# Kernel optimization log

Measured on AMD Instinct MI355X. Metric: run time of the kernel, lower is better.

The kernel has to match this reference:

```python
import jax, jax.numpy as jnp
import numpy as np

EPS = 1e-7  # keras backend epsilon


def _tril_indices(stack_size: int) -> np.ndarray:
    # matches np.nonzero(np.tri(S, S, -1).ravel())[0] in build()
    return np.nonzero(np.tri(stack_size, stack_size, -1).ravel())[0]


def setup_inputs() -> dict:
    key = jax.random.key(0)
    x = jax.random.normal(key, (8, 512, 256), dtype=jnp.float32)
    return {"x": x}


def reference(x) -> jnp.ndarray:
    B, S, D = x.shape
    tril = jnp.asarray(_tril_indices(S))  # static, length S*(S-1)/2
    # pairwise squared L2 over feature dim: (B, S, S, D) -> (B, S, S)
    diff = x[:, :, None, :] - x[:, None, :, :]
    d2 = jnp.sum(jnp.square(diff), axis=-1)
    d = jnp.sqrt(jnp.maximum(d2, EPS))
    # flatten the S x S matrix and gather strict lower-triangular entries
    out = d.reshape(B, S * S)[:, tril]  # (B, S*(S-1)/2)
    return out
```

## Files before the change

kernel.cpp:

```cpp
#include <hip/hip_runtime.h>
#include <hip/hip_bf16.h>
#include <math.h>

#define BB 8
#define SS 512
#define DD 256
#define PP (SS * (SS - 1) / 2)
#define TILES_PER_B (32 * 33 / 2)

typedef short bf16x8 __attribute__((ext_vector_type(8)));
typedef float f32x4 __attribute__((ext_vector_type(4)));

static __device__ inline unsigned short f2bf(float f) {
    unsigned int u = __float_as_uint(f);
    unsigned int r = u + 0x7fffu + ((u >> 16) & 1u);
    return (unsigned short)(r >> 16);
}

__global__ __launch_bounds__(256) void prep_kernel(const float* __restrict__ x,
                                                   unsigned short* __restrict__ xb,
                                                   float* __restrict__ norms) {
    int row  = blockIdx.x * 4 + (threadIdx.x >> 6);
    int lane = threadIdx.x & 63;
    const float4* src = reinterpret_cast<const float4*>(x + (size_t)row * DD) + lane;
    float4 v = *src;
    float ss = v.x * v.x + v.y * v.y + v.z * v.z + v.w * v.w;
    ushort4 pk;
    pk.x = f2bf(v.x); pk.y = f2bf(v.y); pk.z = f2bf(v.z); pk.w = f2bf(v.w);
    *reinterpret_cast<ushort4*>(xb + (size_t)row * DD + lane * 4) = pk;
    #pragma unroll
    for (int o = 32; o > 0; o >>= 1) ss += __shfl_down(ss, o);
    if (lane == 0) norms[row] = ss;
}

__global__ __launch_bounds__(256) void dist_kernel(const unsigned short* __restrict__ xb,
                                                   const float* __restrict__ norms,
                                                   float* __restrict__ out) {
    int w    = blockIdx.x * 4 + (threadIdx.x >> 6);
    int lane = threadIdx.x & 63;
    int b    = w / TILES_PER_B;
    int tidx = w - b * TILES_PER_B;
    int ti = (int)((sqrtf(8.0f * (float)tidx + 1.0f) - 1.0f) * 0.5f);
    while ((ti + 1) * (ti + 2) / 2 <= tidx) ti++;
    while (ti * (ti + 1) / 2 > tidx) ti--;
    int tj = tidx - ti * (ti + 1) / 2;

    int nidx = lane & 15;
    int quad = lane >> 4;

    const unsigned short* arow = xb + ((size_t)(b * SS + ti * 16 + nidx)) * DD + quad * 8;
    const unsigned short* brow = xb + ((size_t)(b * SS + tj * 16 + nidx)) * DD + quad * 8;

    f32x4 acc = {0.f, 0.f, 0.f, 0.f};
    #pragma unroll
    for (int k = 0; k < DD; k += 32) {
        bf16x8 av = *reinterpret_cast<const bf16x8*>(arow + k);
        bf16x8 bv = *reinterpret_cast<const bf16x8*>(brow + k);
        acc = __builtin_amdgcn_mfma_f32_16x16x32_bf16(av, bv, acc, 0, 0, 0);
    }

    int jg = tj * 16 + nidx;
    float nj = norms[b * SS + jg];
    float* outb = out + (size_t)b * PP;
    #pragma unroll
    for (int r = 0; r < 4; r++) {
        int ig = ti * 16 + quad * 4 + r;
        if (ig > jg) {
            float ni = norms[b * SS + ig];
            float d2 = ni + nj - 2.0f * acc[r];
            d2 = fmaxf(d2, 1e-7f);
            outb[(size_t)(ig * (ig - 1) / 2) + jg] = sqrtf(d2);
        }
    }
}

extern "C" void kernel_launch(void* const* d_in, const int* in_sizes, int n_in,
                              void* d_out, int out_size, void* d_ws, size_t ws_size,
                              hipStream_t stream) {
    const float* x = (const float*)d_in[0];
    float* out = (float*)d_out;
    unsigned short* xb = (unsigned short*)d_ws;
    float* norms = (float*)((char*)d_ws + (size_t)BB * SS * DD * 2);

    prep_kernel<<<1024, 256, 0, stream>>>(x, xb, norms);
    dist_kernel<<<1056, 256, 0, stream>>>(xb, norms, out);
}
```

Before: 68.63 us.

## Fuse bf16 conversion and norm computation into distance kernel

```diff
diff --git a/kernel.cpp b/kernel.cpp
--- a/kernel.cpp
+++ b/kernel.cpp
@@ -1,5 +1,4 @@
 #include <hip/hip_runtime.h>
-#include <hip/hip_bf16.h>
 #include <math.h>
 
 #define BB 8
@@ -17,25 +16,22 @@
     return (unsigned short)(r >> 16);
 }
 
-__global__ __launch_bounds__(256) void prep_kernel(const float* __restrict__ x,
-                                                   unsigned short* __restrict__ xb,
-                                                   float* __restrict__ norms) {
-    int row  = blockIdx.x * 4 + (threadIdx.x >> 6);
-    int lane = threadIdx.x & 63;
-    const float4* src = reinterpret_cast<const float4*>(x + (size_t)row * DD) + lane;
-    float4 v = *src;
-    float ss = v.x * v.x + v.y * v.y + v.z * v.z + v.w * v.w;
-    ushort4 pk;
-    pk.x = f2bf(v.x); pk.y = f2bf(v.y); pk.z = f2bf(v.z); pk.w = f2bf(v.w);
-    *reinterpret_cast<ushort4*>(xb + (size_t)row * DD + lane * 4) = pk;
-    #pragma unroll
-    for (int o = 32; o > 0; o >>= 1) ss += __shfl_down(ss, o);
-    if (lane == 0) norms[row] = ss;
+static __device__ inline bf16x8 cvt8(float4 a0, float4 a1) {
+    bf16x8 v;
+    v[0] = (short)f2bf(a0.x); v[1] = (short)f2bf(a0.y);
+    v[2] = (short)f2bf(a0.z); v[3] = (short)f2bf(a0.w);
+    v[4] = (short)f2bf(a1.x); v[5] = (short)f2bf(a1.y);
+    v[6] = (short)f2bf(a1.z); v[7] = (short)f2bf(a1.w);
+    return v;
 }
 
-__global__ __launch_bounds__(256) void dist_kernel(const unsigned short* __restrict__ xb,
-                                                   const float* __restrict__ norms,
-                                                   float* __restrict__ out) {
+static __device__ inline float ssq8(float4 a0, float4 a1) {
+    return a0.x*a0.x + a0.y*a0.y + a0.z*a0.z + a0.w*a0.w
+         + a1.x*a1.x + a1.y*a1.y + a1.z*a1.z + a1.w*a1.w;
+}
+
+__global__ __launch_bounds__(256) void dist_fused(const float* __restrict__ x,
+                                                  float* __restrict__ out) {
     int w    = blockIdx.x * 4 + (threadIdx.x >> 6);
     int lane = threadIdx.x & 63;
     int b    = w / TILES_PER_B;
@@ -48,25 +44,36 @@
     int nidx = lane & 15;
     int quad = lane >> 4;
 
-    const unsigned short* arow = xb + ((size_t)(b * SS + ti * 16 + nidx)) * DD + quad * 8;
-    const unsigned short* brow = xb + ((size_t)(b * SS + tj * 16 + nidx)) * DD + quad * 8;
+    const float* arow = x + ((size_t)(b * SS + ti * 16 + nidx)) * DD + quad * 8;
+    const float* brow = x + ((size_t)(b * SS + tj * 16 + nidx)) * DD + quad * 8;
 
     f32x4 acc = {0.f, 0.f, 0.f, 0.f};
+    float psA = 0.f, psB = 0.f;
     #pragma unroll
     for (int k = 0; k < DD; k += 32) {
-        bf16x8 av = *reinterpret_cast<const bf16x8*>(arow + k);
-        bf16x8 bv = *reinterpret_cast<const bf16x8*>(brow + k);
+        float4 a0 = *reinterpret_cast<const float4*>(arow + k);
+        float4 a1 = *reinterpret_cast<const float4*>(arow + k + 4);
+        float4 b0 = *reinterpret_cast<const float4*>(brow + k);
+        float4 b1 = *reinterpret_cast<const float4*>(brow + k + 4);
+        psA += ssq8(a0, a1);
+        psB += ssq8(b0, b1);
+        bf16x8 av = cvt8(a0, a1);
+        bf16x8 bv = cvt8(b0, b1);
         acc = __builtin_amdgcn_mfma_f32_16x16x32_bf16(av, bv, acc, 0, 0, 0);
     }
 
+    psA += __shfl_xor(psA, 16); psA += __shfl_xor(psA, 32);
+    psB += __shfl_xor(psB, 16); psB += __shfl_xor(psB, 32);
+
     int jg = tj * 16 + nidx;
-    float nj = norms[b * SS + jg];
+    float nj = psB;
     float* outb = out + (size_t)b * PP;
     #pragma unroll
     for (int r = 0; r < 4; r++) {
-        int ig = ti * 16 + quad * 4 + r;
+        int il = quad * 4 + r;
+        int ig = ti * 16 + il;
+        float ni = __shfl(psA, il);
         if (ig > jg) {
-            float ni = norms[b * SS + ig];
             float d2 = ni + nj - 2.0f * acc[r];
             d2 = fmaxf(d2, 1e-7f);
             outb[(size_t)(ig * (ig - 1) / 2) + jg] = sqrtf(d2);
@@ -79,9 +86,6 @@
                               hipStream_t stream) {
     const float* x = (const float*)d_in[0];
     float* out = (float*)d_out;
-    unsigned short* xb = (unsigned short*)d_ws;
-    float* norms = (float*)((char*)d_ws + (size_t)BB * SS * DD * 2);
-
-    prep_kernel<<<1024, 256, 0, stream>>>(x, xb, norms);
-    dist_kernel<<<1056, 256, 0, stream>>>(xb, norms, out);
+    (void)d_ws; (void)ws_size;
+    dist_fused<<<1056, 256, 0, stream>>>(x, out);
 }
```

Measured after the change: 73.79 us. 1.08x slower.

## Compute 32x32 distance blocks per wave with 2x2 MFMA tiles and prefetch

Applied to the files above, without the earlier changes.

```diff
diff --git a/kernel.cpp b/kernel.cpp
--- a/kernel.cpp
+++ b/kernel.cpp
@@ -1,12 +1,12 @@
 #include <hip/hip_runtime.h>
-#include <hip/hip_bf16.h>
 #include <math.h>
 
 #define BB 8
 #define SS 512
 #define DD 256
 #define PP (SS * (SS - 1) / 2)
-#define TILES_PER_B (32 * 33 / 2)
+#define STRIPS 16
+#define SUPER_PER_B (STRIPS * (STRIPS + 1) / 2)
 
 typedef short bf16x8 __attribute__((ext_vector_type(8)));
 typedef float f32x4 __attribute__((ext_vector_type(4)));
@@ -38,38 +38,67 @@
                                                    float* __restrict__ out) {
     int w    = blockIdx.x * 4 + (threadIdx.x >> 6);
     int lane = threadIdx.x & 63;
-    int b    = w / TILES_PER_B;
-    int tidx = w - b * TILES_PER_B;
-    int ti = (int)((sqrtf(8.0f * (float)tidx + 1.0f) - 1.0f) * 0.5f);
-    while ((ti + 1) * (ti + 2) / 2 <= tidx) ti++;
-    while (ti * (ti + 1) / 2 > tidx) ti--;
-    int tj = tidx - ti * (ti + 1) / 2;
+    int b    = w / SUPER_PER_B;
+    int s    = w - b * SUPER_PER_B;
+    int ti = (int)((sqrtf(8.0f * (float)s + 1.0f) - 1.0f) * 0.5f);
+    while ((ti + 1) * (ti + 2) / 2 <= s) ti++;
+    while (ti * (ti + 1) / 2 > s) ti--;
+    int tj = s - ti * (ti + 1) / 2;
 
-    int nidx = lane & 15;
-    int quad = lane >> 4;
+    int r16 = lane & 15;
+    int kq  = lane >> 4;
 
-    const unsigned short* arow = xb + ((size_t)(b * SS + ti * 16 + nidx)) * DD + quad * 8;
-    const unsigned short* brow = xb + ((size_t)(b * SS + tj * 16 + nidx)) * DD + quad * 8;
+    const unsigned short* base = xb + (size_t)b * SS * DD;
+    const unsigned short* a0r = base + (size_t)(ti * 32 + r16) * DD + kq * 8;
+    const unsigned short* a1r = a0r + 16 * DD;
+    const unsigned short* b0r = base + (size_t)(tj * 32 + r16) * DD + kq * 8;
+    const unsigned short* b1r = b0r + 16 * DD;
 
-    f32x4 acc = {0.f, 0.f, 0.f, 0.f};
+    f32x4 acc00 = {0.f,0.f,0.f,0.f}, acc01 = {0.f,0.f,0.f,0.f};
+    f32x4 acc10 = {0.f,0.f,0.f,0.f}, acc11 = {0.f,0.f,0.f,0.f};
+
+    bf16x8 a0 = *reinterpret_cast<const bf16x8*>(a0r);
+    bf16x8 a1 = *reinterpret_cast<const bf16x8*>(a1r);
+    bf16x8 b0 = *reinterpret_cast<const bf16x8*>(b0r);
+    bf16x8 b1 = *reinterpret_cast<const bf16x8*>(b1r);
+
     #pragma unroll
-    for (int k = 0; k < DD; k += 32) {
-        bf16x8 av = *reinterpret_cast<const bf16x8*>(arow + k);
-        bf16x8 bv = *reinterpret_cast<const bf16x8*>(brow + k);
-        acc = __builtin_amdgcn_mfma_f32_16x16x32_bf16(av, bv, acc, 0, 0, 0);
+    for (int k = 32; k <= DD; k += 32) {
+        bf16x8 na0, na1, nb0, nb1;
+        if (k < DD) {
+            na0 = *reinterpret_cast<const bf16x8*>(a0r + k);
+            na1 = *reinterpret_cast<const bf16x8*>(a1r + k);
+            nb0 = *reinterpret_cast<const bf16x8*>(b0r + k);
+            nb1 = *reinterpret_cast<const bf16x8*>(b1r + k);
+        }
+        acc00 = __builtin_amdgcn_mfma_f32_16x16x32_bf16(a0, b0, acc00, 0, 0, 0);
+        acc01 = __builtin_amdgcn_mfma_f32_16x16x32_bf16(a0, b1, acc01, 0, 0, 0);
+        acc10 = __builtin_amdgcn_mfma_f32_16x16x32_bf16(a1, b0, acc10, 0, 0, 0);
+        acc11 = __builtin_amdgcn_mfma_f32_16x16x32_bf16(a1, b1, acc11, 0, 0, 0);
+        if (k < DD) { a0 = na0; a1 = na1; b0 = nb0; b1 = nb1; }
     }
 
-    int jg = tj * 16 + nidx;
-    float nj = norms[b * SS + jg];
+    const float* nrm = norms + b * SS;
     float* outb = out + (size_t)b * PP;
     #pragma unroll
-    for (int r = 0; r < 4; r++) {
-        int ig = ti * 16 + quad * 4 + r;
-        if (ig > jg) {
-            float ni = norms[b * SS + ig];
-            float d2 = ni + nj - 2.0f * acc[r];
-            d2 = fmaxf(d2, 1e-7f);
-            outb[(size_t)(ig * (ig - 1) / 2) + jg] = sqrtf(d2);
+    for (int q = 0; q < 2; q++) {
+        int jg = tj * 32 + q * 16 + r16;
+        float nj = nrm[jg];
+        const f32x4& accq0 = (q == 0) ? acc00 : acc01;
+        const f32x4& accq1 = (q == 0) ? acc10 : acc11;
+        #pragma unroll
+        for (int p = 0; p < 2; p++) {
+            const f32x4& a = (p == 0) ? accq0 : accq1;
+            #pragma unroll
+            for (int r = 0; r < 4; r++) {
+                int ig = ti * 32 + p * 16 + kq * 4 + r;
+                if (ig > jg) {
+                    float ni = nrm[ig];
+                    float d2 = ni + nj - 2.0f * a[r];
+                    d2 = fmaxf(d2, 1e-7f);
+                    outb[(size_t)(ig * (ig - 1) / 2) + jg] = sqrtf(d2);
+                }
+            }
         }
     }
 }
@@ -83,5 +112,5 @@
     float* norms = (float*)((char*)d_ws + (size_t)BB * SS * DD * 2);
 
     prep_kernel<<<1024, 256, 0, stream>>>(x, xb, norms);
-    dist_kernel<<<1056, 256, 0, stream>>>(xb, norms, out);
+    dist_kernel<<<272, 256, 0, stream>>>(xb, norms, out);
 }
```

Result: no change. 69.11 us (+0.7%).
